# Kernel optimization log

Measured on AMD Instinct MI355X. Metric: run time of the kernel, lower is better.

Reference implementation:

```python
import jax, jax.numpy as jnp
import numpy as np

H = 2048  # hidden_size
I = 8192  # intermediate_size
B, S = 4, 2048


def setup_inputs() -> dict:
    key = jax.random.key(0)
    ks = jax.random.split(key, 8)
    scale = 1.0 / np.sqrt(H)
    scale_i = 1.0 / np.sqrt(I)
    x = jax.random.normal(ks[0], (B, S, H), dtype=jnp.float32)
    mask = jax.random.randint(ks[1], (B, S), 0, 2) > 0  # bool per-token routing
    # torch nn.Linear weights are [out_features, in_features]
    w1 = jax.random.normal(ks[2], (I, H), dtype=jnp.float32) * scale
    w2 = jax.random.normal(ks[3], (H, I), dtype=jnp.float32) * scale_i
    w3 = jax.random.normal(ks[4], (I, H), dtype=jnp.float32) * scale
    u1 = jax.random.normal(ks[5], (I, H), dtype=jnp.float32) * scale
    u2 = jax.random.normal(ks[6], (H, I), dtype=jnp.float32) * scale_i
    u3 = jax.random.normal(ks[7], (I, H), dtype=jnp.float32) * scale
    return {"x": x, "mask": mask, "w1": w1, "w2": w2, "w3": w3,
            "u1": u1, "u2": u2, "u3": u3}


def reference(x, mask, w1, w2, w3, u1, u2, u3):
    # branch 1 SwiGLU: silu(x @ w1^T) * (x @ w3^T), then w2
    proj1 = jax.nn.silu(jnp.einsum('bsh,ih->bsi', x, w1)) * jnp.einsum('bsh,ih->bsi', x, w3)
    proj2 = jax.nn.silu(jnp.einsum('bsh,ih->bsi', x, u1)) * jnp.einsum('bsh,ih->bsi', x, u3)
    out1 = jnp.einsum('bsi,hi->bsh', proj1, w2)
    out2 = jnp.einsum('bsi,hi->bsh', proj2, u2)
    m = mask[:, :, None]
    return jnp.where(m, out1, out2)
```

## Files before the change

kernel.cpp:

```cpp
#include <hip/hip_runtime.h>
#include <hip/hip_bf16.h>
#include <stdint.h>

#define DIM_H 2048
#define DIM_I 8192
#define TOKENS 8192
#define RB256 34
#define CROWS (RB256*256)

typedef __attribute__((ext_vector_type(8))) short bf16x8;
typedef __attribute__((ext_vector_type(4))) float f32x4;

#define MF(a,b,c) __builtin_amdgcn_mfma_f32_16x16x32_bf16((a),(b),(c),0,0,0)

__device__ __forceinline__ unsigned short f2bf(float f) {
    union { float f; unsigned u; } v; v.f = f;
    return (unsigned short)((v.u + 0x7FFF + ((v.u >> 16) & 1)) >> 16);
}

__global__ __launch_bounds__(256) void cvt_kernel(const float* __restrict__ in,
                                                  unsigned short* __restrict__ out,
                                                  int n4) {
    int stride = gridDim.x * blockDim.x;
    for (int j = blockIdx.x * blockDim.x + threadIdx.x; j < n4; j += stride) {
        float4 v = reinterpret_cast<const float4*>(in)[j];
        ushort4 o;
        o.x = f2bf(v.x); o.y = f2bf(v.y); o.z = f2bf(v.z); o.w = f2bf(v.w);
        reinterpret_cast<ushort4*>(out)[j] = o;
    }
}

__global__ __launch_bounds__(256) void cvt13_kernel(const float* __restrict__ w1,
                                                    const float* __restrict__ w3,
                                                    unsigned short* __restrict__ W13,
                                                    int n4) {
    int stride = gridDim.x * blockDim.x;
    for (int j = blockIdx.x * blockDim.x + threadIdx.x; j < n4; j += stride) {
        int flat = j << 2;
        int R = flat >> 11;
        int col = flat & 2047;
        int orow = ((R >> 4) << 5) | (R & 15);
        float4 v1 = reinterpret_cast<const float4*>(w1)[j];
        float4 v3 = reinterpret_cast<const float4*>(w3)[j];
        ushort4 o1, o3;
        o1.x=f2bf(v1.x); o1.y=f2bf(v1.y); o1.z=f2bf(v1.z); o1.w=f2bf(v1.w);
        o3.x=f2bf(v3.x); o3.y=f2bf(v3.y); o3.z=f2bf(v3.z); o3.w=f2bf(v3.w);
        *reinterpret_cast<ushort4*>(&W13[(size_t)orow * DIM_H + col]) = o1;
        *reinterpret_cast<ushort4*>(&W13[(size_t)(orow + 16) * DIM_H + col]) = o3;
    }
}

__global__ __launch_bounds__(256) void compact_kernel(const int* __restrict__ mask,
                                                      int* __restrict__ idx,
                                                      int* __restrict__ hdr) {
    __shared__ int cnt[256];
    const int t = threadIdx.x;
    const int base = t * 32;
    unsigned bits = 0;
#pragma unroll
    for (int j = 0; j < 32; ++j)
        if (mask[base + j] != 0) bits |= (1u << j);
    const int c = __popc(bits);
    cnt[t] = c;
    __syncthreads();
    for (int off = 1; off < 256; off <<= 1) {
        int v = cnt[t];
        int add = (t >= off) ? cnt[t - off] : 0;
        __syncthreads();
        cnt[t] = v + add;
        __syncthreads();
    }
    const int Mw  = cnt[255];
    const int MwP = (Mw + 255) & ~255;
    const int Mu  = TOKENS - Mw;
    const int MuP = (Mu + 255) & ~255;

    for (int j = t; j < CROWS; j += 256) idx[j] = -1;
    __syncthreads();

    int pw = cnt[t] - c;
    int pz = base - pw;
#pragma unroll
    for (int j = 0; j < 32; ++j) {
        int tok = base + j;
        if ((bits >> j) & 1) idx[pw++] = tok;
        else                 idx[MwP + pz++] = tok;
    }
    if (t == 0) {
        hdr[0] = MwP >> 8;
        hdr[1] = (MwP + MuP) >> 8;
        hdr[2] = Mw;
        hdr[3] = Mu;
    }
}


#define LDA4(BASE, KS, MQ) do { \
    const unsigned short* _sl = &smem[(BASE) + (KS)*8192]; \
    af0 = *reinterpret_cast<const bf16x8*>(&_sl[(rAb + (MQ)*64 +  0)*32 + c16r]); \
    af1 = *reinterpret_cast<const bf16x8*>(&_sl[(rAb + (MQ)*64 + 16)*32 + c16r]); \
    af2 = *reinterpret_cast<const bf16x8*>(&_sl[(rAb + (MQ)*64 + 32)*32 + c16r]); \
    af3 = *reinterpret_cast<const bf16x8*>(&_sl[(rAb + (MQ)*64 + 48)*32 + c16r]); \
} while(0)

#define LDB4(BASE, KS) do { \
    const unsigned short* _sl = &smem[(BASE) + 16384 + (KS)*8192]; \
    bfr0 = *reinterpret_cast<const bf16x8*>(&_sl[(rBb +  0)*32 + c16r]); \
    bfr1 = *reinterpret_cast<const bf16x8*>(&_sl[(rBb + 16)*32 + c16r]); \
    bfr2 = *reinterpret_cast<const bf16x8*>(&_sl[(rBb + 32)*32 + c16r]); \
    bfr3 = *reinterpret_cast<const bf16x8*>(&_sl[(rBb + 48)*32 + c16r]); \
} while(0)

#define STAGE2(UB_, S0_, S1_, KOFS_) do { \
    __builtin_amdgcn_global_load_lds((const __attribute__((address_space(1))) void*)((S0_) + (KOFS_)), \
        (__attribute__((address_space(3))) void*)&smem[(UB_) + wave*512], 16, 0, 0); \
    __builtin_amdgcn_global_load_lds((const __attribute__((address_space(1))) void*)((S1_) + (KOFS_)), \
        (__attribute__((address_space(3))) void*)&smem[(UB_) + 4096 + wave*512], 16, 0, 0); \
} while(0)

#define MFMA16(M0) do { \
    acc[M0+0][0]=MF(af0,bfr0,acc[M0+0][0]); acc[M0+0][1]=MF(af0,bfr1,acc[M0+0][1]); \
    acc[M0+0][2]=MF(af0,bfr2,acc[M0+0][2]); acc[M0+0][3]=MF(af0,bfr3,acc[M0+0][3]); \
    acc[M0+1][0]=MF(af1,bfr0,acc[M0+1][0]); acc[M0+1][1]=MF(af1,bfr1,acc[M0+1][1]); \
    acc[M0+1][2]=MF(af1,bfr2,acc[M0+1][2]); acc[M0+1][3]=MF(af1,bfr3,acc[M0+1][3]); \
    acc[M0+2][0]=MF(af2,bfr0,acc[M0+2][0]); acc[M0+2][1]=MF(af2,bfr1,acc[M0+2][1]); \
    acc[M0+2][2]=MF(af2,bfr2,acc[M0+2][2]); acc[M0+2][3]=MF(af2,bfr3,acc[M0+2][3]); \
    acc[M0+3][0]=MF(af3,bfr0,acc[M0+3][0]); acc[M0+3][1]=MF(af3,bfr1,acc[M0+3][1]); \
    acc[M0+3][2]=MF(af3,bfr2,acc[M0+3][2]); acc[M0+3][3]=MF(af3,bfr3,acc[M0+3][3]); \
} while(0)

#define BARMFMA(M0) do { \
    __builtin_amdgcn_s_barrier(); \
    __builtin_amdgcn_s_setprio(1); \
    MFMA16(M0); \
    __builtin_amdgcn_s_setprio(0); \
    __builtin_amdgcn_s_barrier(); \
} while(0)

#define KLOOP(NT) do { \
    STAGE2(0,     sa0, sa1, 0);   STAGE2(16384, sb0, sb1, 0); \
    STAGE2(8192,  sa0, sa1, 32);  STAGE2(24576, sb0, sb1, 32); \
    STAGE2(32768, sa0, sa1, 64);  STAGE2(49152, sb0, sb1, 64); \
    asm volatile("s_waitcnt vmcnt(4)" ::: "memory"); \
    __builtin_amdgcn_s_barrier(); \
    int ko = 96; \
    for (int t = 0; t < (NT); ++t) { \
        const int cur = (t & 1) << 15; \
        const int nxt = cur ^ 32768; \
        LDA4(cur, 0, 0); LDB4(cur, 0); STAGE2(nxt + 8192,  sa0, sa1, ko); BARMFMA(0); \
        LDA4(cur, 0, 1);               STAGE2(nxt + 24576, sb0, sb1, ko); BARMFMA(4); \
        LDA4(cur, 1, 0); LDB4(cur, 1); STAGE2(cur,         sa0, sa1, ko + 32); BARMFMA(0); \
        LDA4(cur, 1, 1);               STAGE2(cur + 16384, sb0, sb1, ko + 32); \
        ko += 64; \
        asm volatile("s_waitcnt vmcnt(4)" ::: "memory"); \
        BARMFMA(4); \
    } \
} while(0)

__global__ __launch_bounds__(512, 2) void gemm1_kernel(
    const unsigned short* __restrict__ xb,
    const unsigned short* __restrict__ W13,
    const unsigned short* __restrict__ U13,
    const int* __restrict__ idx, const int* __restrict__ hdr,
    unsigned short* __restrict__ P)
{
    __shared__ __align__(16) unsigned short smem[65536];
    const int wB  = hdr[0];
    const int rbT = hdr[1];
    const int nwg = gridDim.x;
    const int q8  = nwg >> 3;
    const int swz = ((int)blockIdx.x & 7) * q8 + ((int)blockIdx.x >> 3);
    const int rb = swz % RB256;
    const int bx = swz / RB256;
    if (rb >= rbT) return;
    const unsigned short* Bm = (rb < wB) ? W13 : U13;
    const int bm0 = rb << 8;
    const int bn0 = bx << 8;

    const int tid  = threadIdx.x;
    const int lane = tid & 63;
    const int wave = tid >> 6;
    const int wrM = wave >> 2;
    const int wcN = wave & 3;
    const int rAb = wrM * 128 + (lane & 15);
    const int rBb = wcN * 64 + (lane & 15);
    const int c16r = (((lane >> 4) ^ ((lane >> 1) & 3))) << 3;

    const int p0 = tid, p1 = 512 + tid;
    const int r0 = p0 >> 2, r1 = p1 >> 2;
    const int c0 = ((p0 & 3) ^ ((r0 >> 1) & 3)) << 3;
    const int c1 = ((p1 & 3) ^ ((r1 >> 1) & 3)) << 3;
    int t0 = idx[bm0 + r0]; if (t0 < 0) t0 = 0;
    int t1 = idx[bm0 + r1]; if (t1 < 0) t1 = 0;
    const unsigned short* sa0 = xb + (size_t)t0 * DIM_H + c0;
    const unsigned short* sa1 = xb + (size_t)t1 * DIM_H + c1;
    const unsigned short* sb0 = Bm + (size_t)(bn0 + r0) * DIM_H + c0;
    const unsigned short* sb1 = Bm + (size_t)(bn0 + r1) * DIM_H + c1;

    f32x4 acc[8][4] = {};
    bf16x8 af0, af1, af2, af3, bfr0, bfr1, bfr2, bfr3;

    KLOOP(32);

    const int crow = (lane >> 4) << 2;
    const int ccol = lane & 15;
    unsigned short* Pw = P + (size_t)(bm0 + wrM * 128) * DIM_I
                           + (size_t)bx * 128 + wcN * 32 + ccol;
#pragma unroll
    for (int m = 0; m < 8; ++m) {
#pragma unroll
        for (int q = 0; q < 2; ++q) {
            f32x4 h1 = acc[m][2 * q];
            f32x4 h3 = acc[m][2 * q + 1];
#pragma unroll
            for (int r = 0; r < 4; ++r) {
                float a = h1[r];
                float p = a * (1.0f / (1.0f + __expf(-a))) * h3[r];
                Pw[(size_t)(m * 16 + crow + r) * DIM_I + q * 16] = f2bf(p);
            }
        }
    }
}

__global__ __launch_bounds__(512, 2) void gemm2_kernel(
    const unsigned short* __restrict__ P,
    const unsigned short* __restrict__ w2b, const unsigned short* __restrict__ u2b,
    const int* __restrict__ idx, const int* __restrict__ hdr,
    float* __restrict__ out)
{
    __shared__ __align__(16) unsigned short smem[65536];
    const int wB  = hdr[0];
    const int rbT = hdr[1];
    const int nwg = gridDim.x;
    const int q8  = nwg >> 3;
    const int swz = ((int)blockIdx.x & 7) * q8 + ((int)blockIdx.x >> 3);
    const int bx = swz & 7;
    const int rb = swz >> 3;
    if (rb >= rbT) return;
    const unsigned short* Bm = (rb < wB) ? w2b : u2b;
    const int bm0 = rb << 8;
    const int bn0 = bx << 8;

    const int tid  = threadIdx.x;
    const int lane = tid & 63;
    const int wave = tid >> 6;
    const int wrM = wave >> 2;
    const int wcN = wave & 3;
    const int rAb = wrM * 128 + (lane & 15);
    const int rBb = wcN * 64 + (lane & 15);
    const int c16r = (((lane >> 4) ^ ((lane >> 1) & 3))) << 3;

    const int p0 = tid, p1 = 512 + tid;
    const int r0 = p0 >> 2, r1 = p1 >> 2;
    const int c0 = ((p0 & 3) ^ ((r0 >> 1) & 3)) << 3;
    const int c1 = ((p1 & 3) ^ ((r1 >> 1) & 3)) << 3;
    const unsigned short* sa0 = P  + (size_t)(bm0 + r0) * DIM_I + c0;
    const unsigned short* sa1 = P  + (size_t)(bm0 + r1) * DIM_I + c1;
    const unsigned short* sb0 = Bm + (size_t)(bn0 + r0) * DIM_I + c0;
    const unsigned short* sb1 = Bm + (size_t)(bn0 + r1) * DIM_I + c1;

    f32x4 acc[8][4] = {};
    bf16x8 af0, af1, af2, af3, bfr0, bfr1, bfr2, bfr3;

    KLOOP(128);

    const int crow = (lane >> 4) << 2;
    const int ccol = lane & 15;
#pragma unroll
    for (int m = 0; m < 8; ++m) {
#pragma unroll
        for (int r = 0; r < 4; ++r) {
            int rowc = bm0 + wrM * 128 + m * 16 + crow + r;
            int g = idx[rowc];
            if (g >= 0) {
                float* op = out + (size_t)g * DIM_H + bn0 + wcN * 64 + ccol;
#pragma unroll
                for (int n = 0; n < 4; ++n) op[n * 16] = acc[m][n][r];
            }
        }
    }
}

extern "C" void kernel_launch(void* const* d_in, const int* in_sizes, int n_in,
                              void* d_out, int out_size, void* d_ws, size_t ws_size,
                              hipStream_t stream) {
    const float* x    = (const float*)d_in[0];
    const int*   mask = (const int*)d_in[1];
    const float* w1 = (const float*)d_in[2];
    const float* w2 = (const float*)d_in[3];
    const float* w3 = (const float*)d_in[4];
    const float* u1 = (const float*)d_in[5];
    const float* u2 = (const float*)d_in[6];
    const float* u3 = (const float*)d_in[7];
    float* out = (float*)d_out;

    const size_t XN   = (size_t)TOKENS * DIM_H;
    const size_t WN   = (size_t)DIM_I * DIM_H;
    const size_t PN   = (size_t)CROWS * DIM_I;
    const size_t W13N = 2 * WN;

    unsigned short* ws  = (unsigned short*)d_ws;
    unsigned short* xb  = ws;
    unsigned short* Pb  = xb + XN;
    unsigned short* W13 = Pb + PN;
    unsigned short* U13 = W13 + W13N;
    int* idx = (int*)(U13 + W13N);
    int* hdr = idx + CROWS;
    unsigned short* w2b = W13;
    unsigned short* u2b = U13;

    const int cvtBlocks = 2048;
    const int n4 = (int)(WN / 4);

    cvt_kernel  <<<cvtBlocks, 256, 0, stream>>>(x, xb, (int)(XN / 4));
    cvt13_kernel<<<cvtBlocks, 256, 0, stream>>>(w1, w3, W13, n4);
    cvt13_kernel<<<cvtBlocks, 256, 0, stream>>>(u1, u3, U13, n4);
    compact_kernel<<<1, 256, 0, stream>>>(mask, idx, hdr);

    gemm1_kernel<<<64 * RB256, 512, 0, stream>>>(xb, W13, U13, idx, hdr, Pb);

    cvt_kernel<<<cvtBlocks, 256, 0, stream>>>(w2, w2b, n4);
    cvt_kernel<<<cvtBlocks, 256, 0, stream>>>(u2, u2b, n4);

    gemm2_kernel<<<8 * RB256, 512, 0, stream>>>(Pb, w2b, u2b, idx, hdr, out);
}
```

Before: 1.073 ms.

## Restructure GEMM pipelines: fewer barriers in gemm1, 128-row tiles with 3-stage ring in gemm2

gemm1's K-loop now loads all A/B fragments for a 32-wide k-slice at once and issues 32 MFMAs per barrier pair instead of 16, which halves the number of barriers per iteration. gemm2 moves from 256x256 tiles to 128x256 tiles with a triple-buffered LDS ring (larger shared allocation). Each iteration covers 64 k and uses a single barrier, and the grid grows to 8*68 workgroups so more CUs have work. The cost is higher register pressure from holding more fragments, more LDS per block (which may limit occupancy), and reduced reuse of the B operand in gemm2.

```diff
diff --git a/kernel.cpp b/kernel.cpp
--- a/kernel.cpp
+++ b/kernel.cpp
@@ -95,20 +95,12 @@
 }
 
 
-#define LDA4(BASE, KS, MQ) do { \
-    const unsigned short* _sl = &smem[(BASE) + (KS)*8192]; \
-    af0 = *reinterpret_cast<const bf16x8*>(&_sl[(rAb + (MQ)*64 +  0)*32 + c16r]); \
-    af1 = *reinterpret_cast<const bf16x8*>(&_sl[(rAb + (MQ)*64 + 16)*32 + c16r]); \
-    af2 = *reinterpret_cast<const bf16x8*>(&_sl[(rAb + (MQ)*64 + 32)*32 + c16r]); \
-    af3 = *reinterpret_cast<const bf16x8*>(&_sl[(rAb + (MQ)*64 + 48)*32 + c16r]); \
-} while(0)
-
-#define LDB4(BASE, KS) do { \
-    const unsigned short* _sl = &smem[(BASE) + 16384 + (KS)*8192]; \
-    bfr0 = *reinterpret_cast<const bf16x8*>(&_sl[(rBb +  0)*32 + c16r]); \
-    bfr1 = *reinterpret_cast<const bf16x8*>(&_sl[(rBb + 16)*32 + c16r]); \
-    bfr2 = *reinterpret_cast<const bf16x8*>(&_sl[(rBb + 32)*32 + c16r]); \
-    bfr3 = *reinterpret_cast<const bf16x8*>(&_sl[(rBb + 48)*32 + c16r]); \
+#define LDF4(D0,D1,D2,D3, SB, RB) do { \
+    const unsigned short* _sl = &smem[(SB)]; \
+    D0 = *reinterpret_cast<const bf16x8*>(&_sl[((RB) +  0)*32 + c16r]); \
+    D1 = *reinterpret_cast<const bf16x8*>(&_sl[((RB) + 16)*32 + c16r]); \
+    D2 = *reinterpret_cast<const bf16x8*>(&_sl[((RB) + 32)*32 + c16r]); \
+    D3 = *reinterpret_cast<const bf16x8*>(&_sl[((RB) + 48)*32 + c16r]); \
 } while(0)
 
 #define STAGE2(UB_, S0_, S1_, KOFS_) do { \
@@ -118,43 +110,19 @@
         (__attribute__((address_space(3))) void*)&smem[(UB_) + 4096 + wave*512], 16, 0, 0); \
 } while(0)
 
-#define MFMA16(M0) do { \
-    acc[M0+0][0]=MF(af0,bfr0,acc[M0+0][0]); acc[M0+0][1]=MF(af0,bfr1,acc[M0+0][1]); \
-    acc[M0+0][2]=MF(af0,bfr2,acc[M0+0][2]); acc[M0+0][3]=MF(af0,bfr3,acc[M0+0][3]); \
-    acc[M0+1][0]=MF(af1,bfr0,acc[M0+1][0]); acc[M0+1][1]=MF(af1,bfr1,acc[M0+1][1]); \
-    acc[M0+1][2]=MF(af1,bfr2,acc[M0+1][2]); acc[M0+1][3]=MF(af1,bfr3,acc[M0+1][3]); \
-    acc[M0+2][0]=MF(af2,bfr0,acc[M0+2][0]); acc[M0+2][1]=MF(af2,bfr1,acc[M0+2][1]); \
-    acc[M0+2][2]=MF(af2,bfr2,acc[M0+2][2]); acc[M0+2][3]=MF(af2,bfr3,acc[M0+2][3]); \
-    acc[M0+3][0]=MF(af3,bfr0,acc[M0+3][0]); acc[M0+3][1]=MF(af3,bfr1,acc[M0+3][1]); \
-    acc[M0+3][2]=MF(af3,bfr2,acc[M0+3][2]); acc[M0+3][3]=MF(af3,bfr3,acc[M0+3][3]); \
-} while(0)
-
-#define BARMFMA(M0) do { \
-    __builtin_amdgcn_s_barrier(); \
-    __builtin_amdgcn_s_setprio(1); \
-    MFMA16(M0); \
-    __builtin_amdgcn_s_setprio(0); \
-    __builtin_amdgcn_s_barrier(); \
-} while(0)
-
-#define KLOOP(NT) do { \
-    STAGE2(0,     sa0, sa1, 0);   STAGE2(16384, sb0, sb1, 0); \
-    STAGE2(8192,  sa0, sa1, 32);  STAGE2(24576, sb0, sb1, 32); \
-    STAGE2(32768, sa0, sa1, 64);  STAGE2(49152, sb0, sb1, 64); \
-    asm volatile("s_waitcnt vmcnt(4)" ::: "memory"); \
-    __builtin_amdgcn_s_barrier(); \
-    int ko = 96; \
-    for (int t = 0; t < (NT); ++t) { \
-        const int cur = (t & 1) << 15; \
-        const int nxt = cur ^ 32768; \
-        LDA4(cur, 0, 0); LDB4(cur, 0); STAGE2(nxt + 8192,  sa0, sa1, ko); BARMFMA(0); \
-        LDA4(cur, 0, 1);               STAGE2(nxt + 24576, sb0, sb1, ko); BARMFMA(4); \
-        LDA4(cur, 1, 0); LDB4(cur, 1); STAGE2(cur,         sa0, sa1, ko + 32); BARMFMA(0); \
-        LDA4(cur, 1, 1);               STAGE2(cur + 16384, sb0, sb1, ko + 32); \
-        ko += 64; \
-        asm volatile("s_waitcnt vmcnt(4)" ::: "memory"); \
-        BARMFMA(4); \
-    } \
+#define STAGE1(UB_, S0_, KOFS_) \
+    __builtin_amdgcn_global_load_lds((const __attribute__((address_space(1))) void*)((S0_) + (KOFS_)), \
+        (__attribute__((address_space(3))) void*)&smem[(UB_) + wave*512], 16, 0, 0)
+
+#define MFMA32_G1() do { \
+  acc[0][0]=MF(af0,bfr0,acc[0][0]); acc[0][1]=MF(af0,bfr1,acc[0][1]); acc[0][2]=MF(af0,bfr2,acc[0][2]); acc[0][3]=MF(af0,bfr3,acc[0][3]); \
+  acc[1][0]=MF(af1,bfr0,acc[1][0]); acc[1][1]=MF(af1,bfr1,acc[1][1]); acc[1][2]=MF(af1,bfr2,acc[1][2]); acc[1][3]=MF(af1,bfr3,acc[1][3]); \
+  acc[2][0]=MF(af2,bfr0,acc[2][0]); acc[2][1]=MF(af2,bfr1,acc[2][1]); acc[2][2]=MF(af2,bfr2,acc[2][2]); acc[2][3]=MF(af2,bfr3,acc[2][3]); \
+  acc[3][0]=MF(af3,bfr0,acc[3][0]); acc[3][1]=MF(af3,bfr1,acc[3][1]); acc[3][2]=MF(af3,bfr2,acc[3][2]); acc[3][3]=MF(af3,bfr3,acc[3][3]); \
+  acc[4][0]=MF(af4,bfr0,acc[4][0]); acc[4][1]=MF(af4,bfr1,acc[4][1]); acc[4][2]=MF(af4,bfr2,acc[4][2]); acc[4][3]=MF(af4,bfr3,acc[4][3]); \
+  acc[5][0]=MF(af5,bfr0,acc[5][0]); acc[5][1]=MF(af5,bfr1,acc[5][1]); acc[5][2]=MF(af5,bfr2,acc[5][2]); acc[5][3]=MF(af5,bfr3,acc[5][3]); \
+  acc[6][0]=MF(af6,bfr0,acc[6][0]); acc[6][1]=MF(af6,bfr1,acc[6][1]); acc[6][2]=MF(af6,bfr2,acc[6][2]); acc[6][3]=MF(af6,bfr3,acc[6][3]); \
+  acc[7][0]=MF(af7,bfr0,acc[7][0]); acc[7][1]=MF(af7,bfr1,acc[7][1]); acc[7][2]=MF(af7,bfr2,acc[7][2]); acc[7][3]=MF(af7,bfr3,acc[7][3]); \
 } while(0)
 
 __global__ __launch_bounds__(512, 2) void gemm1_kernel(
@@ -198,9 +166,42 @@
     const unsigned short* sb1 = Bm + (size_t)(bn0 + r1) * DIM_H + c1;
 
     f32x4 acc[8][4] = {};
-    bf16x8 af0, af1, af2, af3, bfr0, bfr1, bfr2, bfr3;
-
-    KLOOP(32);
+    bf16x8 af0, af1, af2, af3, af4, af5, af6, af7, bfr0, bfr1, bfr2, bfr3;
+
+    STAGE2(0,     sa0, sa1, 0);
+    STAGE2(16384, sb0, sb1, 0);
+    STAGE2(8192,  sa0, sa1, 32);
+    STAGE2(24576, sb0, sb1, 32);
+    STAGE2(32768, sa0, sa1, 64);
+    STAGE2(49152, sb0, sb1, 64);
+    asm volatile("s_waitcnt vmcnt(8)" ::: "memory");
+    __builtin_amdgcn_s_barrier();
+    int ko = 96;
+    for (int t = 0; t < 32; ++t) {
+        const int cur = (t & 1) << 15;
+        const int nxt = cur ^ 32768;
+        LDF4(af0,af1,af2,af3, cur,          rAb);
+        LDF4(af4,af5,af6,af7, cur,          rAb + 64);
+        LDF4(bfr0,bfr1,bfr2,bfr3, cur + 16384, rBb);
+        STAGE2(nxt + 8192,  sa0, sa1, ko);
+        STAGE2(nxt + 24576, sb0, sb1, ko);
+        __builtin_amdgcn_s_setprio(1);
+        MFMA32_G1();
+        __builtin_amdgcn_s_setprio(0);
+        asm volatile("s_waitcnt vmcnt(8)" ::: "memory");
+        __builtin_amdgcn_s_barrier();
+        LDF4(af0,af1,af2,af3, cur + 8192,   rAb);
+        LDF4(af4,af5,af6,af7, cur + 8192,   rAb + 64);
+        LDF4(bfr0,bfr1,bfr2,bfr3, cur + 24576, rBb);
+        STAGE2(cur,         sa0, sa1, ko + 32);
+        STAGE2(cur + 16384, sb0, sb1, ko + 32);
+        ko += 64;
+        __builtin_amdgcn_s_setprio(1);
+        MFMA32_G1();
+        __builtin_amdgcn_s_setprio(0);
+        asm volatile("s_waitcnt vmcnt(8)" ::: "memory");
+        __builtin_amdgcn_s_barrier();
+    }
 
     const int crow = (lane >> 4) << 2;
     const int ccol = lane & 15;
@@ -222,23 +223,30 @@
     }
 }
 
+#define MFMA16Q(AF0,AF1,AF2,AF3, B0,B1,B2,B3) do { \
+  acc[0][0]=MF(AF0,B0,acc[0][0]); acc[0][1]=MF(AF0,B1,acc[0][1]); acc[0][2]=MF(AF0,B2,acc[0][2]); acc[0][3]=MF(AF0,B3,acc[0][3]); \
+  acc[1][0]=MF(AF1,B0,acc[1][0]); acc[1][1]=MF(AF1,B1,acc[1][1]); acc[1][2]=MF(AF1,B2,acc[1][2]); acc[1][3]=MF(AF1,B3,acc[1][3]); \
+  acc[2][0]=MF(AF2,B0,acc[2][0]); acc[2][1]=MF(AF2,B1,acc[2][1]); acc[2][2]=MF(AF2,B2,acc[2][2]); acc[2][3]=MF(AF2,B3,acc[2][3]); \
+  acc[3][0]=MF(AF3,B0,acc[3][0]); acc[3][1]=MF(AF3,B1,acc[3][1]); acc[3][2]=MF(AF3,B2,acc[3][2]); acc[3][3]=MF(AF3,B3,acc[3][3]); \
+} while(0)
+
 __global__ __launch_bounds__(512, 2) void gemm2_kernel(
     const unsigned short* __restrict__ P,
     const unsigned short* __restrict__ w2b, const unsigned short* __restrict__ u2b,
     const int* __restrict__ idx, const int* __restrict__ hdr,
     float* __restrict__ out)
 {
-    __shared__ __align__(16) unsigned short smem[65536];
-    const int wB  = hdr[0];
-    const int rbT = hdr[1];
+    __shared__ __align__(16) unsigned short smem[73728];
+    const int wB2  = hdr[0] * 2;
+    const int rbT2 = hdr[1] * 2;
     const int nwg = gridDim.x;
     const int q8  = nwg >> 3;
     const int swz = ((int)blockIdx.x & 7) * q8 + ((int)blockIdx.x >> 3);
-    const int bx = swz & 7;
-    const int rb = swz >> 3;
-    if (rb >= rbT) return;
-    const unsigned short* Bm = (rb < wB) ? w2b : u2b;
-    const int bm0 = rb << 8;
+    const int rb = swz % 68;
+    const int bx = swz / 68;
+    if (rb >= rbT2) return;
+    const unsigned short* Bm = (rb < wB2) ? w2b : u2b;
+    const int bm0 = rb << 7;
     const int bn0 = bx << 8;
 
     const int tid  = threadIdx.x;
@@ -246,31 +254,60 @@
     const int wave = tid >> 6;
     const int wrM = wave >> 2;
     const int wcN = wave & 3;
-    const int rAb = wrM * 128 + (lane & 15);
+    const int rAb = wrM * 64 + (lane & 15);
     const int rBb = wcN * 64 + (lane & 15);
     const int c16r = (((lane >> 4) ^ ((lane >> 1) & 3))) << 3;
 
-    const int p0 = tid, p1 = 512 + tid;
-    const int r0 = p0 >> 2, r1 = p1 >> 2;
-    const int c0 = ((p0 & 3) ^ ((r0 >> 1) & 3)) << 3;
-    const int c1 = ((p1 & 3) ^ ((r1 >> 1) & 3)) << 3;
+    const int r0 = tid >> 2, r1 = 128 + r0;
+    const int c0 = ((tid & 3) ^ ((r0 >> 1) & 3)) << 3;
+    const int c1 = ((tid & 3) ^ ((r1 >> 1) & 3)) << 3;
     const unsigned short* sa0 = P  + (size_t)(bm0 + r0) * DIM_I + c0;
-    const unsigned short* sa1 = P  + (size_t)(bm0 + r1) * DIM_I + c1;
     const unsigned short* sb0 = Bm + (size_t)(bn0 + r0) * DIM_I + c0;
     const unsigned short* sb1 = Bm + (size_t)(bn0 + r1) * DIM_I + c1;
 
-    f32x4 acc[8][4] = {};
-    bf16x8 af0, af1, af2, af3, bfr0, bfr1, bfr2, bfr3;
-
-    KLOOP(128);
+    f32x4 acc[4][4] = {};
+    bf16x8 af0, af1, af2, af3, af4, af5, af6, af7;
+    bf16x8 bfr0, bfr1, bfr2, bfr3, bfr4, bfr5, bfr6, bfr7;
+
+    STAGE1(0,     sa0, 0);
+    STAGE1(4096,  sa0, 32);
+    STAGE2(8192,  sb0, sb1, 0);
+    STAGE2(16384, sb0, sb1, 32);
+    STAGE1(24576,         sa0, 64);
+    STAGE1(24576 + 4096,  sa0, 96);
+    STAGE2(24576 + 8192,  sb0, sb1, 64);
+    STAGE2(24576 + 16384, sb0, sb1, 96);
+    asm volatile("s_waitcnt vmcnt(6)" ::: "memory");
+    __builtin_amdgcn_s_barrier();
+    int ko = 128, cb = 0;
+    for (int t = 0; t < 128; ++t) {
+        const int base = cb * 24576;
+        int nb = base + 49152; if (nb >= 73728) nb -= 73728;
+        LDF4(af0,af1,af2,af3,     base,          rAb);
+        LDF4(af4,af5,af6,af7,     base + 4096,   rAb);
+        LDF4(bfr0,bfr1,bfr2,bfr3, base + 8192,   rBb);
+        LDF4(bfr4,bfr5,bfr6,bfr7, base + 16384,  rBb);
+        STAGE1(nb,         sa0, ko);
+        STAGE1(nb + 4096,  sa0, ko + 32);
+        STAGE2(nb + 8192,  sb0, sb1, ko);
+        STAGE2(nb + 16384, sb0, sb1, ko + 32);
+        ko += 64;
+        __builtin_amdgcn_s_setprio(1);
+        MFMA16Q(af0,af1,af2,af3, bfr0,bfr1,bfr2,bfr3);
+        MFMA16Q(af4,af5,af6,af7, bfr4,bfr5,bfr6,bfr7);
+        __builtin_amdgcn_s_setprio(0);
+        asm volatile("s_waitcnt vmcnt(6)" ::: "memory");
+        __builtin_amdgcn_s_barrier();
+        cb = (cb == 2) ? 0 : cb + 1;
+    }
 
     const int crow = (lane >> 4) << 2;
     const int ccol = lane & 15;
 #pragma unroll
-    for (int m = 0; m < 8; ++m) {
+    for (int m = 0; m < 4; ++m) {
 #pragma unroll
         for (int r = 0; r < 4; ++r) {
-            int rowc = bm0 + wrM * 128 + m * 16 + crow + r;
+            int rowc = bm0 + wrM * 64 + m * 16 + crow + r;
             int g = idx[rowc];
             if (g >= 0) {
                 float* op = out + (size_t)g * DIM_H + bn0 + wcN * 64 + ccol;
@@ -322,5 +359,5 @@
     cvt_kernel<<<cvtBlocks, 256, 0, stream>>>(w2, w2b, n4);
     cvt_kernel<<<cvtBlocks, 256, 0, stream>>>(u2, u2b, n4);
 
-    gemm2_kernel<<<8 * RB256, 512, 0, stream>>>(Pb, w2b, u2b, idx, hdr, out);
-}
+    gemm2_kernel<<<8 * 68, 512, 0, stream>>>(Pb, w2b, u2b, idx, hdr, out);
+}
```

Result: no change. 1.056 ms (-1.6%).

## Restructure GEMM k-loop into four full-tile phases with one barrier each

Applied to the files above, without the earlier changes.

Each phase of the shared k-loop now loads all eight A fragments and four B fragments at once, issues the next global-to-LDS stage, runs 32 MFMAs, and then does a single vmcnt wait plus barrier. Before, each k-step was split into half-tile MFMA groups, each wrapped in two barriers. The aim is to cut barrier count and give more MFMA work between synchronisations, at the cost of more live fragment registers. The gemm2 block index mapping also changes to walk row blocks first, which alters L2 reuse of the weight tiles.

```diff
diff --git a/kernel.cpp b/kernel.cpp
--- a/kernel.cpp
+++ b/kernel.cpp
@@ -95,20 +95,12 @@
 }
 
 
-#define LDA4(BASE, KS, MQ) do { \
-    const unsigned short* _sl = &smem[(BASE) + (KS)*8192]; \
-    af0 = *reinterpret_cast<const bf16x8*>(&_sl[(rAb + (MQ)*64 +  0)*32 + c16r]); \
-    af1 = *reinterpret_cast<const bf16x8*>(&_sl[(rAb + (MQ)*64 + 16)*32 + c16r]); \
-    af2 = *reinterpret_cast<const bf16x8*>(&_sl[(rAb + (MQ)*64 + 32)*32 + c16r]); \
-    af3 = *reinterpret_cast<const bf16x8*>(&_sl[(rAb + (MQ)*64 + 48)*32 + c16r]); \
-} while(0)
-
-#define LDB4(BASE, KS) do { \
-    const unsigned short* _sl = &smem[(BASE) + 16384 + (KS)*8192]; \
-    bfr0 = *reinterpret_cast<const bf16x8*>(&_sl[(rBb +  0)*32 + c16r]); \
-    bfr1 = *reinterpret_cast<const bf16x8*>(&_sl[(rBb + 16)*32 + c16r]); \
-    bfr2 = *reinterpret_cast<const bf16x8*>(&_sl[(rBb + 32)*32 + c16r]); \
-    bfr3 = *reinterpret_cast<const bf16x8*>(&_sl[(rBb + 48)*32 + c16r]); \
+#define LDF4(D0,D1,D2,D3, SB, RB) do { \
+    const unsigned short* _sl = &smem[(SB)]; \
+    D0 = *reinterpret_cast<const bf16x8*>(&_sl[((RB) +  0)*32 + c16r]); \
+    D1 = *reinterpret_cast<const bf16x8*>(&_sl[((RB) + 16)*32 + c16r]); \
+    D2 = *reinterpret_cast<const bf16x8*>(&_sl[((RB) + 32)*32 + c16r]); \
+    D3 = *reinterpret_cast<const bf16x8*>(&_sl[((RB) + 48)*32 + c16r]); \
 } while(0)
 
 #define STAGE2(UB_, S0_, S1_, KOFS_) do { \
@@ -118,42 +110,47 @@
         (__attribute__((address_space(3))) void*)&smem[(UB_) + 4096 + wave*512], 16, 0, 0); \
 } while(0)
 
-#define MFMA16(M0) do { \
-    acc[M0+0][0]=MF(af0,bfr0,acc[M0+0][0]); acc[M0+0][1]=MF(af0,bfr1,acc[M0+0][1]); \
-    acc[M0+0][2]=MF(af0,bfr2,acc[M0+0][2]); acc[M0+0][3]=MF(af0,bfr3,acc[M0+0][3]); \
-    acc[M0+1][0]=MF(af1,bfr0,acc[M0+1][0]); acc[M0+1][1]=MF(af1,bfr1,acc[M0+1][1]); \
-    acc[M0+1][2]=MF(af1,bfr2,acc[M0+1][2]); acc[M0+1][3]=MF(af1,bfr3,acc[M0+1][3]); \
-    acc[M0+2][0]=MF(af2,bfr0,acc[M0+2][0]); acc[M0+2][1]=MF(af2,bfr1,acc[M0+2][1]); \
-    acc[M0+2][2]=MF(af2,bfr2,acc[M0+2][2]); acc[M0+2][3]=MF(af2,bfr3,acc[M0+2][3]); \
-    acc[M0+3][0]=MF(af3,bfr0,acc[M0+3][0]); acc[M0+3][1]=MF(af3,bfr1,acc[M0+3][1]); \
-    acc[M0+3][2]=MF(af3,bfr2,acc[M0+3][2]); acc[M0+3][3]=MF(af3,bfr3,acc[M0+3][3]); \
-} while(0)
-
-#define BARMFMA(M0) do { \
+#define MFMA32() do { \
+  __builtin_amdgcn_s_setprio(1); \
+  acc[0][0]=MF(af0,bfr0,acc[0][0]); acc[0][1]=MF(af0,bfr1,acc[0][1]); acc[0][2]=MF(af0,bfr2,acc[0][2]); acc[0][3]=MF(af0,bfr3,acc[0][3]); \
+  acc[1][0]=MF(af1,bfr0,acc[1][0]); acc[1][1]=MF(af1,bfr1,acc[1][1]); acc[1][2]=MF(af1,bfr2,acc[1][2]); acc[1][3]=MF(af1,bfr3,acc[1][3]); \
+  acc[2][0]=MF(af2,bfr0,acc[2][0]); acc[2][1]=MF(af2,bfr1,acc[2][1]); acc[2][2]=MF(af2,bfr2,acc[2][2]); acc[2][3]=MF(af2,bfr3,acc[2][3]); \
+  acc[3][0]=MF(af3,bfr0,acc[3][0]); acc[3][1]=MF(af3,bfr1,acc[3][1]); acc[3][2]=MF(af3,bfr2,acc[3][2]); acc[3][3]=MF(af3,bfr3,acc[3][3]); \
+  acc[4][0]=MF(af4,bfr0,acc[4][0]); acc[4][1]=MF(af4,bfr1,acc[4][1]); acc[4][2]=MF(af4,bfr2,acc[4][2]); acc[4][3]=MF(af4,bfr3,acc[4][3]); \
+  acc[5][0]=MF(af5,bfr0,acc[5][0]); acc[5][1]=MF(af5,bfr1,acc[5][1]); acc[5][2]=MF(af5,bfr2,acc[5][2]); acc[5][3]=MF(af5,bfr3,acc[5][3]); \
+  acc[6][0]=MF(af6,bfr0,acc[6][0]); acc[6][1]=MF(af6,bfr1,acc[6][1]); acc[6][2]=MF(af6,bfr2,acc[6][2]); acc[6][3]=MF(af6,bfr3,acc[6][3]); \
+  acc[7][0]=MF(af7,bfr0,acc[7][0]); acc[7][1]=MF(af7,bfr1,acc[7][1]); acc[7][2]=MF(af7,bfr2,acc[7][2]); acc[7][3]=MF(af7,bfr3,acc[7][3]); \
+  __builtin_amdgcn_s_setprio(0); \
+} while(0)
+
+#define VMB() do { \
+    asm volatile("s_waitcnt vmcnt(8)" ::: "memory"); \
     __builtin_amdgcn_s_barrier(); \
-    __builtin_amdgcn_s_setprio(1); \
-    MFMA16(M0); \
-    __builtin_amdgcn_s_setprio(0); \
-    __builtin_amdgcn_s_barrier(); \
+} while(0)
+
+#define PHASE(ABASE, BBASE, SA_UB, SB_UB, KO) do { \
+    LDF4(af0,af1,af2,af3, (ABASE), rAb); \
+    LDF4(af4,af5,af6,af7, (ABASE), rAb + 64); \
+    LDF4(bfr0,bfr1,bfr2,bfr3, (BBASE), rBb); \
+    STAGE2((SA_UB), sa0, sa1, (KO)); \
+    STAGE2((SB_UB), sb0, sb1, (KO)); \
+    MFMA32(); \
+    VMB(); \
 } while(0)
 
 #define KLOOP(NT) do { \
-    STAGE2(0,     sa0, sa1, 0);   STAGE2(16384, sb0, sb1, 0); \
-    STAGE2(8192,  sa0, sa1, 32);  STAGE2(24576, sb0, sb1, 32); \
-    STAGE2(32768, sa0, sa1, 64);  STAGE2(49152, sb0, sb1, 64); \
-    asm volatile("s_waitcnt vmcnt(4)" ::: "memory"); \
-    __builtin_amdgcn_s_barrier(); \
-    int ko = 96; \
-    for (int t = 0; t < (NT); ++t) { \
-        const int cur = (t & 1) << 15; \
-        const int nxt = cur ^ 32768; \
-        LDA4(cur, 0, 0); LDB4(cur, 0); STAGE2(nxt + 8192,  sa0, sa1, ko); BARMFMA(0); \
-        LDA4(cur, 0, 1);               STAGE2(nxt + 24576, sb0, sb1, ko); BARMFMA(4); \
-        LDA4(cur, 1, 0); LDB4(cur, 1); STAGE2(cur,         sa0, sa1, ko + 32); BARMFMA(0); \
-        LDA4(cur, 1, 1);               STAGE2(cur + 16384, sb0, sb1, ko + 32); \
-        ko += 64; \
-        asm volatile("s_waitcnt vmcnt(4)" ::: "memory"); \
-        BARMFMA(4); \
+    STAGE2(0,     sa0, sa1, 0);   STAGE2(16384, sb0, sb1, 0);    \
+    STAGE2(8192,  sa0, sa1, 32);  STAGE2(24576, sb0, sb1, 32);   \
+    STAGE2(32768, sa0, sa1, 64);  STAGE2(49152, sb0, sb1, 64);   \
+    VMB(); \
+    for (int s = 0; s < (NT)/2; ++s) { \
+         \
+        PHASE(0,             16384,         32768 + 8192,  32768 + 24576, 96);    \
+        PHASE(8192,          24576,         0,             16384,         128);   \
+         \
+        PHASE(32768,         32768 + 16384, 8192,          24576,         160);   \
+        PHASE(32768 + 8192,  32768 + 24576, 32768,         32768 + 16384, 192);   \
+        sa0 += 128; sa1 += 128; sb0 += 128; sb1 += 128; \
     } \
 } while(0)
 
@@ -169,9 +166,9 @@
     const int rbT = hdr[1];
     const int nwg = gridDim.x;
     const int q8  = nwg >> 3;
-    const int swz = ((int)blockIdx.x & 7) * q8 + ((int)blockIdx.x >> 3);
-    const int rb = swz % RB256;
-    const int bx = swz / RB256;
+    const int swzb = ((int)blockIdx.x & 7) * q8 + ((int)blockIdx.x >> 3);
+    const int rb = swzb % RB256;
+    const int bx = swzb / RB256;
     if (rb >= rbT) return;
     const unsigned short* Bm = (rb < wB) ? W13 : U13;
     const int bm0 = rb << 8;
@@ -198,7 +195,7 @@
     const unsigned short* sb1 = Bm + (size_t)(bn0 + r1) * DIM_H + c1;
 
     f32x4 acc[8][4] = {};
-    bf16x8 af0, af1, af2, af3, bfr0, bfr1, bfr2, bfr3;
+    bf16x8 af0, af1, af2, af3, af4, af5, af6, af7, bfr0, bfr1, bfr2, bfr3;
 
     KLOOP(32);
 
@@ -233,9 +230,9 @@
     const int rbT = hdr[1];
     const int nwg = gridDim.x;
     const int q8  = nwg >> 3;
-    const int swz = ((int)blockIdx.x & 7) * q8 + ((int)blockIdx.x >> 3);
-    const int bx = swz & 7;
-    const int rb = swz >> 3;
+    const int swzb = ((int)blockIdx.x & 7) * q8 + ((int)blockIdx.x >> 3);
+    const int rb = swzb % RB256;
+    const int bx = swzb / RB256;
     if (rb >= rbT) return;
     const unsigned short* Bm = (rb < wB) ? w2b : u2b;
     const int bm0 = rb << 8;
@@ -260,7 +257,7 @@
     const unsigned short* sb1 = Bm + (size_t)(bn0 + r1) * DIM_I + c1;
 
     f32x4 acc[8][4] = {};
-    bf16x8 af0, af1, af2, af3, bfr0, bfr1, bfr2, bfr3;
+    bf16x8 af0, af1, af2, af3, af4, af5, af6, af7, bfr0, bfr1, bfr2, bfr3;
 
     KLOOP(128);
 
```

Measured after the change: 1.099 ms. +2.4%, slower.
